# Kernel tuning notes

Hardware: AMD Instinct MI355X
Metric: run time of the kernel (lower is better)

## Reference

```python
import jax, jax.numpy as jnp
import numpy as np

KERNEL = 3          # conv kernel size (stride 1)
NUM_SEG = 512       # static cap on number of pooled segments (pad semantics)
NEG = -10.0         # fill value for positions not covered by the strided conv


def _sinusoidal_pe(S, D):
    pos = np.arange(S)[:, None].astype(np.float32)
    div = np.exp(-np.log(10000.0) * (np.arange(0, D, 2).astype(np.float32) / D))
    pe = np.zeros((S, D), dtype=np.float32)
    pe[:, 0::2] = np.sin(pos * div)
    pe[:, 1::2] = np.cos(pos * div)
    return jnp.asarray(pe)


def setup_inputs() -> dict:
    key = jax.random.key(0)
    B, L, D = 8, 2048, 1024
    Ch = D // KERNEL  # 341
    ks = jax.random.split(key, 4)
    hidden = jax.random.normal(ks[0], (B, L, D), jnp.float32)
    lengths = jax.random.randint(ks[1], (B,), L // 2, L + 1)
    attention_mask = (jnp.arange(L)[None, :] < lengths[:, None]).astype(jnp.float32)
    w1 = jax.random.normal(ks[2], (Ch, D, KERNEL), jnp.float32) / np.sqrt(D * KERNEL)
    b1 = jnp.zeros((Ch,), jnp.float32)
    w2 = jax.random.normal(ks[3], (1, Ch, 1), jnp.float32) / np.sqrt(Ch)
    b2 = jnp.full((1,), -2.5, jnp.float32)  # init_for_12 bias
    return {"hidden": hidden, "attention_mask": attention_mask,
            "w1": w1, "b1": b1, "w2": w2, "b2": b2}


def reference(hidden, attention_mask, w1, b1, w2, b2):
    B, L, D = hidden.shape
    dt = hidden.dtype
    # --- strided-conv boundary logits (eval path, no Gumbel noise) ---
    x = jnp.swapaxes(hidden, 1, 2)  # (B, D, L)
    h = jax.lax.conv_general_dilated(x, w1, (1,), 'VALID',
                                     dimension_numbers=('NCH', 'OIH', 'NCH'))
    h = jax.nn.relu(h + b1[None, :, None])            # (B, Ch, L-2)
    strided = jnp.einsum('bcl,oc->bl', h, w2[:, :, 0]) + b2[0]  # (B, L-2)
    # scatter strided logits to positions kernel-1 + i (i.e. [2:L])
    logits = jnp.full((B, L), NEG, dt).at[:, KERNEL - 1:].set(strided)
    probs = jax.nn.sigmoid(logits)
    soft = probs
    hard_samp = (probs > 0.5).astype(dt)
    hard = hard_samp + soft - jax.lax.stop_gradient(soft)  # straight-through
    # --- mask and force a boundary at the last real token ---
    hard = hard * attention_mask
    pad = attention_mask == 0
    first_pad = pad & (jnp.cumsum(pad.astype(jnp.int32), axis=1) == 1)
    last_real = jnp.roll(first_pad, -1, axis=1).at[:, -1].set(False).astype(dt)
    hard = jnp.maximum(hard, last_real)
    # --- dynamic downsample: mean-pool tokens within boundary segments ---
    seg = jnp.cumsum(hard, axis=1) - hard  # segment id per token (B, L)
    sid = jnp.arange(NUM_SEG, dtype=dt)
    foo = 1.0 - jnp.clip(jnp.abs(sid[None, None, :] - seg[:, :, None]), 0.0, 1.0)  # (B,L,S)
    foo = foo * attention_mask[:, :, None]
    lel = foo / (jnp.sum(foo, axis=1, keepdims=True) + 1e-9)
    pooled = jnp.einsum('bls,bld->bsd', lel, hidden)  # (B, S, D)
    pooled = pooled + _sinusoidal_pe(NUM_SEG, D)[None].astype(dt)
    # --- shortened attention mask (stream compaction of kept positions) ---
    keep = jax.lax.stop_gradient(hard) > 0.5
    order = jnp.argsort(jnp.logical_not(keep).astype(jnp.int32), axis=1)  # stable: kept first
    gathered = jnp.take_along_axis(attention_mask, order, axis=1)[:, :NUM_SEG]
    n_keep = jnp.sum(keep, axis=1)
    valid = jnp.arange(NUM_SEG)[None, :] < n_keep[:, None]
    short_mask = jnp.where(valid, gathered, 0.0)
    num_boundaries = jnp.sum(hard)
    total_positions = jnp.sum(attention_mask)
    return pooled, num_boundaries, total_positions, short_mask
```

## Files before the change

kernel.cpp:

```cpp
#include <hip/hip_runtime.h>
#include <hip/hip_bf16.h>
#include <cmath>

#define B_SZ 8
#define L_SZ 2048
#define D_SZ 1024
#define CH 341
#define CP 384
#define LCONV 2046
#define NSEG 512
#define KDIM 3072
#define KSTEPS 48
#define NCHUNK 128
#define W1XB 576

#define POOLED_N (B_SZ * NSEG * D_SZ)

typedef _Float16 f16x8 __attribute__((ext_vector_type(8)));
typedef _Float16 f16x4 __attribute__((ext_vector_type(4)));
typedef float f32x4 __attribute__((ext_vector_type(4)));

__device__ __forceinline__ void gl_lds16(const void* g, void* l) {
    __builtin_amdgcn_global_load_lds(
        (const __attribute__((address_space(1))) unsigned int*)g,
        (__attribute__((address_space(3))) unsigned int*)l, 16, 0, 0);
}

__global__ __launch_bounds__(256) void convert_all_kernel(
        const float* __restrict__ hidden, _Float16* __restrict__ hid16,
        const float* __restrict__ w1, const float* __restrict__ b2,
        _Float16* __restrict__ bfrag, float* __restrict__ logits,
        float* __restrict__ chunksum) {
    const int bx = blockIdx.x, b = blockIdx.y;
    const int tid = threadIdx.x;
    if (bx < NCHUNK) {
        const int d0 = tid * 4;
        const float* src = hidden + ((size_t)b * L_SZ + bx * 16) * D_SZ + d0;
        _Float16* dst = hid16 + ((size_t)b * L_SZ + bx * 16) * D_SZ + d0;
        float4 acc = make_float4(0.f, 0.f, 0.f, 0.f);
        #pragma unroll
        for (int r = 0; r < 16; ++r) {
            float4 v = *(const float4*)(src + (size_t)r * D_SZ);
            acc.x += v.x; acc.y += v.y; acc.z += v.z; acc.w += v.w;
            f16x4 o;
            o[0] = (_Float16)v.x; o[1] = (_Float16)v.y;
            o[2] = (_Float16)v.z; o[3] = (_Float16)v.w;
            *(f16x4*)(dst + (size_t)r * D_SZ) = o;
        }
        *(float4*)(chunksum + ((size_t)(b * NCHUNK + bx)) * D_SZ + d0) = acc;
    } else {
        int idx = (((bx - NCHUNK) * B_SZ) + b) * 256 + tid;
        int j = idx & 7;
        int lane = (idx >> 3) & 63;
        int kc = (idx >> 9) & 1;
        int rest = idx >> 10;
        int s = rest % KSTEPS;
        int tt = rest / KSTEPS;
        int c = tt * 16 + (lane & 15);
        int k = s * 64 + kc * 32 + ((lane >> 4) << 3) + j;
        int kk = k >> 10, d = k & 1023;
        float v = (c < CH) ? w1[((size_t)c * 1024 + d) * 3 + kk] : 0.0f;
        bfrag[idx] = (_Float16)v;
        if (idx < B_SZ * LCONV) logits[idx] = b2[0];
    }
}

#define LDS_BUF 8192

__global__ __launch_bounds__(256, 2) void conv_mfma_kernel(
        const _Float16* __restrict__ hid16, const _Float16* __restrict__ bfrag,
        const float* __restrict__ b1, const float* __restrict__ w2,
        float* __restrict__ logits) {
    const int nt = blockIdx.x;
    const int mt = blockIdx.y;
    const int b  = blockIdx.z;
    const int l0 = mt * 64;
    const int n0 = nt * 192;
    const int tid = threadIdx.x;
    const int wave = tid >> 6, lane = tid & 63;
    const int wn = wave;
    const int quad = lane >> 4, l16 = lane & 15;

    __shared__ __align__(16) char lds[2 * LDS_BUF];

    const _Float16* hb = hid16 + (size_t)b * L_SZ * D_SZ;

    const _Float16* pa[2];
    #pragma unroll
    for (int p = 0; p < 2; ++p) {
        int f = p * 256 + tid;
        int kc = f >> 8, e = f & 255;
        int m = ((e >> 6) << 4) + (e & 15);
        int koff = ((e >> 4) & 3) * 8;
        int l = l0 + m; if (l > LCONV - 1) l = LCONV - 1;
        pa[p] = hb + (size_t)l * 1024 + kc * 32 + koff;
    }

    const f16x8* bp = (const f16x8*)bfrag;
    const f16x8* bptr[3];
    #pragma unroll
    for (int jj = 0; jj < 3; ++jj) {
        int tt = nt * 12 + wn * 3 + jj;
        bptr[jj] = bp + (size_t)tt * (KSTEPS * 2 * 64) + lane;
    }

    f32x4 acc[4][3] = {};
    f16x8 bc[3][2], bn[3][2];

    #pragma unroll
    for (int jj = 0; jj < 3; ++jj)
        #pragma unroll
        for (int kc = 0; kc < 2; ++kc)
            bc[jj][kc] = bptr[jj][kc * 64];
    #pragma unroll
    for (int jj = 0; jj < 3; ++jj) bptr[jj] += 128;
    #pragma unroll
    for (int p = 0; p < 2; ++p)
        gl_lds16(pa[p], lds + (p * 256 + wave * 64) * 16);
    #pragma unroll
    for (int p = 0; p < 2; ++p) pa[p] += 64;
    __syncthreads();

    int cur = 0;
    for (int s = 0; s < KSTEPS - 1; ++s) {
        const int nxt = cur ^ LDS_BUF;
        #pragma unroll
        for (int jj = 0; jj < 3; ++jj)
            #pragma unroll
            for (int kc = 0; kc < 2; ++kc)
                bn[jj][kc] = bptr[jj][kc * 64];
        #pragma unroll
        for (int jj = 0; jj < 3; ++jj) bptr[jj] += 128;
        #pragma unroll
        for (int p = 0; p < 2; ++p)
            gl_lds16(pa[p], lds + nxt + (p * 256 + wave * 64) * 16);
        #pragma unroll
        for (int p = 0; p < 2; ++p) pa[p] += 64;

        #pragma unroll
        for (int kc = 0; kc < 2; ++kc) {
            f16x8 a[4];
            #pragma unroll
            for (int ii = 0; ii < 4; ++ii)
                a[ii] = *(const f16x8*)(lds + cur + (kc * 256 + ii * 64 + lane) * 16);
            #pragma unroll
            for (int ii = 0; ii < 4; ++ii)
                #pragma unroll
                for (int jj = 0; jj < 3; ++jj)
                    acc[ii][jj] = __builtin_amdgcn_mfma_f32_16x16x32_f16(
                        a[ii], bc[jj][kc], acc[ii][jj], 0, 0, 0);
        }
        __syncthreads();
        #pragma unroll
        for (int jj = 0; jj < 3; ++jj)
            #pragma unroll
            for (int kc = 0; kc < 2; ++kc)
                bc[jj][kc] = bn[jj][kc];
        cur = nxt;
    }
    #pragma unroll
    for (int kc = 0; kc < 2; ++kc) {
        f16x8 a[4];
        #pragma unroll
        for (int ii = 0; ii < 4; ++ii)
            a[ii] = *(const f16x8*)(lds + cur + (kc * 256 + ii * 64 + lane) * 16);
        #pragma unroll
        for (int ii = 0; ii < 4; ++ii)
            #pragma unroll
            for (int jj = 0; jj < 3; ++jj)
                acc[ii][jj] = __builtin_amdgcn_mfma_f32_16x16x32_f16(
                    a[ii], bc[jj][kc], acc[ii][jj], 0, 0, 0);
    }
    __syncthreads();

    float cb1[3], cw2[3];
    #pragma unroll
    for (int jj = 0; jj < 3; ++jj) {
        int ch = n0 + wn * 48 + jj * 16 + l16;
        bool v = ch < CH;
        cb1[jj] = v ? b1[ch] : 0.0f;
        cw2[jj] = v ? w2[ch] : 0.0f;
    }
    float* red = (float*)lds;
    #pragma unroll
    for (int ii = 0; ii < 4; ++ii)
        #pragma unroll
        for (int r = 0; r < 4; ++r) {
            float P = 0.0f;
            #pragma unroll
            for (int jj = 0; jj < 3; ++jj) {
                float h = acc[ii][jj][r] + cb1[jj];
                if (h > 0.0f) P += h * cw2[jj];
            }
            P += __shfl_xor(P, 1);
            P += __shfl_xor(P, 2);
            P += __shfl_xor(P, 4);
            P += __shfl_xor(P, 8);
            if (l16 == 0)
                red[(ii * 16 + quad * 4 + r) * 4 + wn] = P;
        }
    __syncthreads();
    if (tid < 64) {
        int l = l0 + tid;
        if (l < LCONV)
            atomicAdd(&logits[b * LCONV + l],
                      red[tid * 4] + red[tid * 4 + 1] + red[tid * 4 + 2] + red[tid * 4 + 3]);
    }
}

__global__ __launch_bounds__(256) void scanfix_kernel(
        const float* __restrict__ logits, const float* __restrict__ amask,
        const float* __restrict__ hidden, const float* __restrict__ w1,
        const float* __restrict__ b1, const float* __restrict__ w2,
        const float* __restrict__ b2,
        int* __restrict__ segstart, float* __restrict__ scratch,
        float* __restrict__ short_mask) {
    const int b = blockIdx.x, tid = threadIdx.x;
    __shared__ float slog[2048];
    __shared__ float hrow[3 * 1024];
    __shared__ int sdata[256];
    __shared__ float sred[256];
    __shared__ int flags[64];
    __shared__ int nflag;
    __shared__ int s_len, s_total;

    for (int t = tid; t < LCONV; t += 256)
        slog[t] = logits[b * LCONV + t];
    if (tid == 0) nflag = 0;

    int cnt = 0;
    #pragma unroll
    for (int j = 0; j < 8; ++j) {
        int l = tid * 8 + j;
        cnt += (amask[b * L_SZ + l] > 0.5f) ? 1 : 0;
    }
    sdata[tid] = cnt; __syncthreads();
    for (int off = 128; off > 0; off >>= 1) {
        if (tid < off) sdata[tid] += sdata[tid + off];
        __syncthreads();
    }
    if (tid == 0) s_len = sdata[0];
    __syncthreads();
    const int len = s_len;

    for (int t = tid; t < LCONV; t += 256)
        if (fabsf(slog[t]) < 0.02f) {
            int k = atomicAdd(&nflag, 1);
            if (k < 64) flags[k] = t;
        }
    __syncthreads();
    const int nf = (nflag < 64) ? nflag : 64;
    for (int fi = 0; fi < nf; ++fi) {
        const int l = flags[fi];
        for (int t = tid; t < 3072; t += 256)
            hrow[t] = hidden[((size_t)b * L_SZ + l) * 1024 + t];
        __syncthreads();
        float tot = 0.0f;
        for (int c = tid; c < CH; c += 256) {
            const float* wr = w1 + (size_t)c * 3072;
            float dot = 0.0f;
            for (int d = 0; d < 1024; ++d)
                dot += hrow[d] * wr[d * 3] + hrow[1024 + d] * wr[d * 3 + 1]
                     + hrow[2048 + d] * wr[d * 3 + 2];
            float h = dot + b1[c];
            if (h > 0.0f) tot += h * w2[c];
        }
        sred[tid] = tot; __syncthreads();
        for (int off = 128; off > 0; off >>= 1) {
            if (tid < off) sred[tid] += sred[tid + off];
            __syncthreads();
        }
        if (tid == 0) slog[l] = sred[0] + b2[0];
        __syncthreads();
    }

    int bits[8]; int tsum = 0;
    #pragma unroll
    for (int j = 0; j < 8; ++j) {
        int l = tid * 8 + j;
        int h = 0;
        if (l >= 2 && l < len) h = (slog[l - 2] > 0.0f) ? 1 : 0;
        if (len < L_SZ && l == len - 1) h = 1;
        bits[j] = h; tsum += h;
    }
    __syncthreads();
    sdata[tid] = tsum; __syncthreads();
    for (int off = 1; off < 256; off <<= 1) {
        int v = (tid >= off) ? sdata[tid - off] : 0;
        __syncthreads();
        sdata[tid] += v;
        __syncthreads();
    }
    const int texcl = sdata[tid] - tsum;
    if (tid == 255) s_total = sdata[255];
    __syncthreads();
    const int total = s_total;

    for (int s = tid; s <= NSEG; s += 256)
        segstart[b * (NSEG + 1) + s] = (s == 0) ? 0 : len;
    __syncthreads();
    int run = texcl;
    #pragma unroll
    for (int j = 0; j < 8; ++j) {
        int l = tid * 8 + j;
        if (bits[j]) {
            if (run + 1 <= NSEG) segstart[b * (NSEG + 1) + run + 1] = l + 1;
            run++;
        }
    }

    if (tid == 0) {
        scratch[b] = (float)total;
        scratch[B_SZ + b] = (float)len;
    }
    for (int s = tid; s < NSEG; s += 256)
        short_mask[b * NSEG + s] = (s < total) ? 1.0f : 0.0f;
}

__global__ __launch_bounds__(256) void pool_gather_kernel(
        const float* __restrict__ hidden, const float* __restrict__ chunksum,
        const int* __restrict__ segstart, const float* __restrict__ scratch,
        float* __restrict__ pooled,
        float* __restrict__ out_nb, float* __restrict__ out_tp) {
    const int s = blockIdx.x, b = blockIdx.y, tid = threadIdx.x;
    if (s == 0 && b == 0 && tid == 0) {
        float nb = 0.f, tp = 0.f;
        #pragma unroll
        for (int i = 0; i < B_SZ; ++i) { nb += scratch[i]; tp += scratch[B_SZ + i]; }
        *out_nb = nb; *out_tp = tp;
    }
    const int l0 = segstart[b * (NSEG + 1) + s];
    const int l1 = segstart[b * (NSEG + 1) + s + 1];
    const int d0 = tid * 4;
    float4 a = make_float4(0.f, 0.f, 0.f, 0.f);
    if (l1 > l0) {
        const int cF = (l0 + 15) >> 4;
        const int cL = l1 >> 4;
        const float* hb = hidden + (size_t)b * L_SZ * D_SZ + d0;
        if (cL > cF) {
            const float* cs = chunksum + ((size_t)b * NCHUNK) * D_SZ + d0;
            int c = cF;
            for (; c + 3 < cL; c += 4) {
                float4 v0 = *(const float4*)(cs + (size_t)c * D_SZ);
                float4 v1 = *(const float4*)(cs + (size_t)(c + 1) * D_SZ);
                float4 v2 = *(const float4*)(cs + (size_t)(c + 2) * D_SZ);
                float4 v3 = *(const float4*)(cs + (size_t)(c + 3) * D_SZ);
                a.x += v0.x + v1.x + v2.x + v3.x;
                a.y += v0.y + v1.y + v2.y + v3.y;
                a.z += v0.z + v1.z + v2.z + v3.z;
                a.w += v0.w + v1.w + v2.w + v3.w;
            }
            for (; c < cL; ++c) {
                float4 v = *(const float4*)(cs + (size_t)c * D_SZ);
                a.x += v.x; a.y += v.y; a.z += v.z; a.w += v.w;
            }
            for (int l = l0; l < cF * 16; ++l) {
                float4 v = *(const float4*)(hb + (size_t)l * D_SZ);
                a.x += v.x; a.y += v.y; a.z += v.z; a.w += v.w;
            }
            for (int l = cL * 16; l < l1; ++l) {
                float4 v = *(const float4*)(hb + (size_t)l * D_SZ);
                a.x += v.x; a.y += v.y; a.z += v.z; a.w += v.w;
            }
        } else {
            for (int l = l0; l < l1; ++l) {
                float4 v = *(const float4*)(hb + (size_t)l * D_SZ);
                a.x += v.x; a.y += v.y; a.z += v.z; a.w += v.w;
            }
        }
    }
    const float inv = 1.0f / ((float)(l1 - l0) + 1e-9f);
    const float ce = -9.210340371976184f / 512.0f;
    const int i = d0 >> 1;
    const float t0 = (float)s * expf(ce * (float)i);
    const float t1 = (float)s * expf(ce * (float)(i + 1));
    float4 out;
    out.x = a.x * inv + sinf(t0);
    out.y = a.y * inv + cosf(t0);
    out.z = a.z * inv + sinf(t1);
    out.w = a.w * inv + cosf(t1);
    *(float4*)(pooled + ((size_t)(b * NSEG + s)) * D_SZ + d0) = out;
}

extern "C" void kernel_launch(void* const* d_in, const int* in_sizes, int n_in,
                              void* d_out, int out_size, void* d_ws, size_t ws_size,
                              hipStream_t stream) {
    const float* hidden = (const float*)d_in[0];
    const float* amask  = (const float*)d_in[1];
    const float* w1     = (const float*)d_in[2];
    const float* b1     = (const float*)d_in[3];
    const float* w2     = (const float*)d_in[4];
    const float* b2     = (const float*)d_in[5];

    float* out    = (float*)d_out;
    float* pooled = out;
    float* nb     = out + POOLED_N;
    float* tp     = nb + 1;
    float* smask  = out + POOLED_N + 2;

    const size_t HID_E = (size_t)B_SZ * L_SZ * D_SZ;
    const size_t OFF_HID16    = 0;
    const size_t OFF_BPACK    = OFF_HID16 + HID_E * 2;
    const size_t OFF_LOGITS   = OFF_BPACK + (size_t)CP * KDIM * 2;
    const size_t OFF_SEGSTART = OFF_LOGITS + (size_t)B_SZ * LCONV * 4;
    const size_t OFF_SCRATCH  = OFF_SEGSTART + (size_t)B_SZ * (NSEG + 1) * 4;
    const size_t OFF_CHUNKSUM = OFF_SCRATCH + 1024;

    _Float16* hid16   = (_Float16*)((char*)d_ws + OFF_HID16);
    _Float16* bfrag   = (_Float16*)((char*)d_ws + OFF_BPACK);
    float*    logits  = (float*)((char*)d_ws + OFF_LOGITS);
    int*      segst   = (int*)((char*)d_ws + OFF_SEGSTART);
    float*    scratch = (float*)((char*)d_ws + OFF_SCRATCH);
    float*    chsum   = (float*)((char*)d_ws + OFF_CHUNKSUM);

    convert_all_kernel<<<dim3(NCHUNK + W1XB, B_SZ), 256, 0, stream>>>(
        hidden, hid16, w1, b2, bfrag, logits, chsum);
    conv_mfma_kernel<<<dim3(2, 32, B_SZ), 256, 0, stream>>>(hid16, bfrag, b1, w2, logits);
    scanfix_kernel<<<B_SZ, 256, 0, stream>>>(logits, amask, hidden, w1, b1, w2, b2,
                                             segst, scratch, smask);
    pool_gather_kernel<<<dim3(NSEG, B_SZ), 256, 0, stream>>>(hidden, chsum, segst,
                                                             scratch, pooled, nb, tp);
}
```

Before: 199.7 us.

## Give each wave private LDS A-tiles and pipeline loads with vmcnt waits instead of barriers

Each wave now loads its own full 64-row A tile into a private double-buffered LDS region (64KB total) and uses explicit s_waitcnt vmcnt counts rather than block-wide __syncthreads, with B fragments double-buffered in registers two steps ahead. This removes per-step barriers and deepens prefetch. The cost is four times more global->LDS traffic for A, since each wave redundantly loads the shared tile, and 64KB of LDS per block may limit occupancy below the two blocks per CU the launch bounds request. There is also a correctness risk: LDS reads issued right after the vmcnt wait may not be safely ordered against the global_load_lds writes.

New measurement: 255.4 us. 27.9% more time.

```diff
diff --git a/kernel.cpp b/kernel.cpp
--- a/kernel.cpp
+++ b/kernel.cpp
@@ -65,7 +65,38 @@
     }
 }
 
-#define LDS_BUF 8192
+#define WAITV14() asm volatile("s_waitcnt vmcnt(14)" ::: "memory")
+#define WAITV0()  asm volatile("s_waitcnt vmcnt(0)" ::: "memory")
+
+#define LOAD_B(DST) do {                                                    \
+    _Pragma("unroll")                                                       \
+    for (int jj = 0; jj < 3; ++jj) {                                        \
+        DST[jj][0] = bptr[jj][0];                                           \
+        DST[jj][1] = bptr[jj][64];                                          \
+        bptr[jj] += 128;                                                    \
+    } } while (0)
+
+#define ISSUE_A(BUF) do {                                                   \
+    _Pragma("unroll")                                                       \
+    for (int q = 0; q < 8; ++q) {                                           \
+        gl_lds16(pa[q], (BUF) + q * 1024);                                  \
+        pa[q] += 64;                                                        \
+    } } while (0)
+
+#define COMPUTE(BUF, BSET) do {                                             \
+    _Pragma("unroll")                                                       \
+    for (int kc = 0; kc < 2; ++kc) {                                        \
+        f16x8 a[4];                                                         \
+        _Pragma("unroll")                                                   \
+        for (int ii = 0; ii < 4; ++ii)                                      \
+            a[ii] = *(const f16x8*)((BUF) + (kc * 256 + ii * 64 + lane) * 16); \
+        _Pragma("unroll")                                                   \
+        for (int ii = 0; ii < 4; ++ii)                                      \
+            _Pragma("unroll")                                               \
+            for (int jj = 0; jj < 3; ++jj)                                  \
+                acc[ii][jj] = __builtin_amdgcn_mfma_f32_16x16x32_f16(       \
+                    a[ii], BSET[jj][kc], acc[ii][jj], 0, 0, 0);             \
+    } } while (0)
 
 __global__ __launch_bounds__(256, 2) void conv_mfma_kernel(
         const _Float16* __restrict__ hid16, const _Float16* __restrict__ bfrag,
@@ -81,19 +112,18 @@
     const int wn = wave;
     const int quad = lane >> 4, l16 = lane & 15;
 
-    __shared__ __align__(16) char lds[2 * LDS_BUF];
+    __shared__ __align__(16) char lds[65536];
+    char* buf0 = lds + wave * 16384;
+    char* buf1 = buf0 + 8192;
 
     const _Float16* hb = hid16 + (size_t)b * L_SZ * D_SZ;
 
-    const _Float16* pa[2];
-    #pragma unroll
-    for (int p = 0; p < 2; ++p) {
-        int f = p * 256 + tid;
-        int kc = f >> 8, e = f & 255;
-        int m = ((e >> 6) << 4) + (e & 15);
-        int koff = ((e >> 4) & 3) * 8;
+    const _Float16* pa[8];
+    #pragma unroll
+    for (int q = 0; q < 8; ++q) {
+        int m = (q & 3) * 16 + (lane & 15);
         int l = l0 + m; if (l > LCONV - 1) l = LCONV - 1;
-        pa[p] = hb + (size_t)l * 1024 + kc * 32 + koff;
+        pa[q] = hb + (size_t)l * 1024 + (q >> 2) * 32 + (lane >> 4) * 8;
     }
 
     const f16x8* bp = (const f16x8*)bfrag;
@@ -105,72 +135,24 @@
     }
 
     f32x4 acc[4][3] = {};
-    f16x8 bc[3][2], bn[3][2];
-
-    #pragma unroll
-    for (int jj = 0; jj < 3; ++jj)
-        #pragma unroll
-        for (int kc = 0; kc < 2; ++kc)
-            bc[jj][kc] = bptr[jj][kc * 64];
-    #pragma unroll
-    for (int jj = 0; jj < 3; ++jj) bptr[jj] += 128;
-    #pragma unroll
-    for (int p = 0; p < 2; ++p)
-        gl_lds16(pa[p], lds + (p * 256 + wave * 64) * 16);
-    #pragma unroll
-    for (int p = 0; p < 2; ++p) pa[p] += 64;
-    __syncthreads();
-
-    int cur = 0;
-    for (int s = 0; s < KSTEPS - 1; ++s) {
-        const int nxt = cur ^ LDS_BUF;
-        #pragma unroll
-        for (int jj = 0; jj < 3; ++jj)
-            #pragma unroll
-            for (int kc = 0; kc < 2; ++kc)
-                bn[jj][kc] = bptr[jj][kc * 64];
-        #pragma unroll
-        for (int jj = 0; jj < 3; ++jj) bptr[jj] += 128;
-        #pragma unroll
-        for (int p = 0; p < 2; ++p)
-            gl_lds16(pa[p], lds + nxt + (p * 256 + wave * 64) * 16);
-        #pragma unroll
-        for (int p = 0; p < 2; ++p) pa[p] += 64;
-
-        #pragma unroll
-        for (int kc = 0; kc < 2; ++kc) {
-            f16x8 a[4];
-            #pragma unroll
-            for (int ii = 0; ii < 4; ++ii)
-                a[ii] = *(const f16x8*)(lds + cur + (kc * 256 + ii * 64 + lane) * 16);
-            #pragma unroll
-            for (int ii = 0; ii < 4; ++ii)
-                #pragma unroll
-                for (int jj = 0; jj < 3; ++jj)
-                    acc[ii][jj] = __builtin_amdgcn_mfma_f32_16x16x32_f16(
-                        a[ii], bc[jj][kc], acc[ii][jj], 0, 0, 0);
-        }
-        __syncthreads();
-        #pragma unroll
-        for (int jj = 0; jj < 3; ++jj)
-            #pragma unroll
-            for (int kc = 0; kc < 2; ++kc)
-                bc[jj][kc] = bn[jj][kc];
-        cur = nxt;
-    }
-    #pragma unroll
-    for (int kc = 0; kc < 2; ++kc) {
-        f16x8 a[4];
-        #pragma unroll
-        for (int ii = 0; ii < 4; ++ii)
-            a[ii] = *(const f16x8*)(lds + cur + (kc * 256 + ii * 64 + lane) * 16);
-        #pragma unroll
-        for (int ii = 0; ii < 4; ++ii)
-            #pragma unroll
-            for (int jj = 0; jj < 3; ++jj)
-                acc[ii][jj] = __builtin_amdgcn_mfma_f32_16x16x32_f16(
-                    a[ii], bc[jj][kc], acc[ii][jj], 0, 0, 0);
-    }
+    f16x8 B0[3][2], B1[3][2];
+
+    LOAD_B(B0); ISSUE_A(buf0);
+    LOAD_B(B1); ISSUE_A(buf1);
+
+    for (int t = 0; t < 23; ++t) {
+        WAITV14();
+        COMPUTE(buf0, B0);
+        LOAD_B(B0); ISSUE_A(buf0);
+        WAITV14();
+        COMPUTE(buf1, B1);
+        LOAD_B(B1); ISSUE_A(buf1);
+    }
+    WAITV14();
+    COMPUTE(buf0, B0);
+    WAITV0();
+    COMPUTE(buf1, B1);
+
     __syncthreads();
 
     float cb1[3], cw2[3];
```
